# Kernel tuning notes

Measured on AMD Instinct MI355X. Metric: run time of the kernel, lower is better.

## Reference

```python
import jax, jax.numpy as jnp
import numpy as np

B, S, E, NH = 2, 2048, 1024, 4
HD = E // NH  # 256


def setup_inputs() -> dict:
    key = jax.random.key(0)
    ks = jax.random.split(key, 8)
    return {
        "q": jax.random.normal(ks[0], (B, S, E), jnp.float32),
        "k": jax.random.normal(ks[1], (B, S, E), jnp.float32),
        "v": jax.random.normal(ks[2], (B, S, E), jnp.float32),
        # gate Dense params (kernel zero-init in the module; use small random for a nontrivial baseline)
        "igate_kernel": jax.random.normal(ks[3], (3 * E, NH), jnp.float32) * 0.02,
        "igate_bias": jax.random.normal(ks[4], (NH,), jnp.float32) * 0.1,
        "fgate_kernel": jax.random.normal(ks[5], (3 * E, NH), jnp.float32) * 0.02,
        "fgate_bias": jnp.linspace(3.0, 6.0, NH, dtype=jnp.float32),  # bias_linspace_init
        "rms_scale": jax.random.normal(ks[6], (HD,), jnp.float32) * 0.02,
    }


def _mlstm_head(q, k, v, ig, fg, eps=1e-06):
    # q,k,v: (S, DH); ig, fg: (S, 1)
    s, dh = q.shape
    log_f = jax.nn.log_sigmoid(fg)                       # (S,1)
    cs = jnp.concatenate([jnp.zeros((1, 1), log_f.dtype),
                          jnp.cumsum(log_f, axis=0)], axis=0)  # (S+1,1)
    neg = jnp.asarray(-0.7 * jnp.finfo(cs.dtype).max, cs.dtype)
    log_d = jnp.where(jnp.tri(s, dtype=bool),
                      (cs - cs.T)[1:, 1:] + ig.T, neg)   # (S,S)
    m = jnp.max(log_d, axis=-1, keepdims=True)           # row-wise stabilizer
    d = jnp.exp(log_d - m)
    c = (q @ (k.T / jnp.sqrt(dh))) * d                   # (S,S)
    n = jnp.maximum(jnp.sum(c, axis=-1, keepdims=True), jnp.exp(-m))
    return (c / (n + eps)) @ v                           # (S,DH)


def reference(q, k, v, igate_kernel, igate_bias, fgate_kernel, fgate_bias, rms_scale):
    b, s, e = q.shape
    nh = igate_kernel.shape[1]
    hd = e // nh
    gate_in = jnp.concatenate((q, k, v), axis=-1)                 # (B,S,3E)
    ig = (gate_in @ igate_kernel + igate_bias).swapaxes(-1, -2)[..., None]  # (B,NH,S,1)
    fg = (gate_in @ fgate_kernel + fgate_bias).swapaxes(-1, -2)[..., None]  # (B,NH,S,1)
    qh = q.reshape(b, s, nh, hd).swapaxes(1, 2)                   # (B,NH,S,HD)
    kh = k.reshape(b, s, nh, hd).swapaxes(1, 2)
    vh = v.reshape(b, s, nh, hd).swapaxes(1, 2)
    h = jax.vmap(jax.vmap(_mlstm_head))(qh, kh, vh, ig, fg)      # (B,NH,S,HD)
    # RMSNorm over head_dim with (1+scale)
    var = jnp.mean(jnp.square(h.astype(jnp.float32)), axis=-1, keepdims=True)
    h = (h * jax.lax.rsqrt(var + 1e-06)).astype(h.dtype) * (1.0 + rms_scale)
    return h.swapaxes(1, 2).reshape(b, s, e)
```

## Files before the change

### kernel.cpp

```cpp
#include <hip/hip_runtime.h>
#include <math.h>

static constexpr int B_  = 2;
static constexpr int S_  = 2048;
static constexpr int E_  = 1024;
static constexpr int NH_ = 4;
static constexpr int HD_ = 256;
static constexpr int BH_ = B_ * NH_;

typedef __attribute__((ext_vector_type(8))) _Float16 half8;
typedef __attribute__((ext_vector_type(4))) float    f32x4;
typedef __attribute__((ext_vector_type(4))) _Float16 half4v;


__device__ __forceinline__ int wofs(int e) { return (e << 4) ^ ((e & 0x38) << 1); }

__global__ __launch_bounds__(1024) void prep_kernel(
    const float* __restrict__ q, const float* __restrict__ k, const float* __restrict__ v,
    const float* __restrict__ igk, const float* __restrict__ igb,
    const float* __restrict__ fgk, const float* __restrict__ fgb,
    float* __restrict__ ig_out, float* __restrict__ fg_out,
    _Float16* __restrict__ Qh, _Float16* __restrict__ Kh, _Float16* __restrict__ Vt)
{
    __shared__ __align__(16) char PSM[98304];
// ... 23 lines not shown
        const int e4 = l * 4 + 256 * j;
        float4 g4;
        if (j < 4)       g4 = *(const float4*)(qrow + e4);
        else if (j < 8)  g4 = *(const float4*)(krow + (e4 - E_));
        else             g4 = *(const float4*)(vrow + (e4 - 2 * E_));
        const float ge[4] = {g4.x, g4.y, g4.z, g4.w};
        if (j < 4) {
            const int d = e4 & 255, hh = e4 >> 8;
            const int idx = ((s >> 4) * 8 + (d >> 5)) * 512
                          + (s & 15) * 8 + (((d & 31) >> 3) << 7) + (d & 7);
            half4v st;
            st.x = (_Float16)(ge[0] * 0.0625f); st.y = (_Float16)(ge[1] * 0.0625f);
            st.z = (_Float16)(ge[2] * 0.0625f); st.w = (_Float16)(ge[3] * 0.0625f);
            *(half4v*)(Qh + ((size_t)(b * NH_ + hh)) * (S_ * HD_) + idx) = st;
        } else if (j < 8) {
            const int e2 = e4 - E_;
            const int d = e2 & 255, hh = e2 >> 8;
            const int idx = ((s >> 4) * 8 + (d >> 5)) * 512
                          + (s & 15) * 8 + (((d & 31) >> 3) << 7) + (d & 7);
            half4v st;
            st.x = (_Float16)ge[0]; st.y = (_Float16)ge[1];
            st.z = (_Float16)ge[2]; st.w = (_Float16)ge[3];
            *(half4v*)(Kh + ((size_t)(b * NH_ + hh)) * (S_ * HD_) + idx) = st;
        }
        #pragma unroll
        for (int i = 0; i < 4; ++i) {
            float4 wiv = *(const float4*)(wiB + wofs(e4 + i));
            float4 wfv = *(const float4*)(wfB + wofs(e4 + i));
            accI[0] = fmaf(ge[i], wiv.x, accI[0]); accI[1] = fmaf(ge[i], wiv.y, accI[1]);
            accI[2] = fmaf(ge[i], wiv.z, accI[2]); accI[3] = fmaf(ge[i], wiv.w, accI[3]);
            accF[0] = fmaf(ge[i], wfv.x, accF[0]); accF[1] = fmaf(ge[i], wfv.y, accF[1]);
            accF[2] = fmaf(ge[i], wfv.z, accF[2]); accF[3] = fmaf(ge[i], wfv.w, accF[3]);
        }
    }
    #pragma unroll
    for (int m = 1; m < 64; m <<= 1) {
        #pragma unroll
        for (int h = 0; h < 4; ++h) {
            accI[h] += __shfl_xor(accI[h], m);
            accF[h] += __shfl_xor(accF[h], m);
        }
    }
    if (l == 0) {
        #pragma unroll
        for (int h = 0; h < 4; ++h) {
            ig_out[((size_t)(b * NH_ + h)) * S_ + s] = accI[h] + igb[h];
            fg_out[((size_t)(b * NH_ + h)) * S_ + s] = accF[h] + fgb[h];
        }
    }

    __syncthreads();
    {
        float (*tile)[65] = (float(*)[65])(PSM + (t >> 8) * 16640);
        const int tid = t & 255;
        const int m  = blockIdx.x * 4 + (t >> 8);
        const int bh = m & 7;
        const int sb = (m >> 3) & 31;
        const int db = m >> 8;
        const int bb = bh >> 2, hh = bh & 3;
        const int j4 = (tid & 15) * 4;
        const int i0 = tid >> 4;
        const float* src = v + ((size_t)(bb * S_ + sb * 64)) * E_ + hh * HD_ + db * 64;
        #pragma unroll
        for (int p = 0; p < 4; ++p) {
            int i = i0 + p * 16;
            float4 val = *(const float4*)(src + (size_t)i * E_ + j4);
            tile[i][j4] = val.x; tile[i][j4+1] = val.y; tile[i][j4+2] = val.z; tile[i][j4+3] = val.w;
        }
        __syncthreads();
        const int ll = tid & 63;
        const int sw_ = tid >> 6;
        _Float16* dstb = Vt + (size_t)bh * (S_ * HD_);
        #pragma unroll
        for (int kb = 0; kb < 2; ++kb) {
            half8 pk;
            #pragma unroll
            for (int jj = 0; jj < 8; ++jj)
                pk[jj] = (_Float16)tile[kb * 32 + (ll >> 4) * 8 + jj][sw_ * 16 + (ll & 15)];
            *(half8*)(dstb + ((size_t)((sb * 16 + db * 4 + sw_) * 2 + kb)) * 512 + ll * 8) = pk;
        }
    }
}

static constexpr int OFF_AMM = 16384;
static constexpr int OFF_G   = OFF_AMM + S_ * 4;
static constexpr int OFF_M   = OFF_G + S_ * 4;
static constexpr int OFF_RS  = OFF_M + S_ * 4;
static constexpr int OFF_SS  = OFF_RS + 1024;
static constexpr int OFF_WR  = OFF_SS + 1024;
static constexpr int SMB     = OFF_WR + 64;

#define TILE_BODY(KFC, KFN)                                                   \
{                                                                             \
                  \
    const _Float16* vb_ = Vtp + (size_t)jt * 32768 + l * 8;                   \
    _Pragma("unroll")                                                         \
    for (int dn = 0; dn < 2; ++dn) {                                          \
        _Pragma("unroll")                                                     \
        for (int k0 = 0; k0 < 4; ++k0)                                        \
            vf[dn * 4 + k0] = *(const half8*)(vb_                             \
                + (((k0 >> 1) * 16 + w * 2 + dn) * 2 + (k0 & 1)) * 512);      \
    }                                                                         \
           \
    if (jt + 1 < Tt) {                                                        \
        const _Float16* kb_ = Kp + ((size_t)((jt + 1) * 8 + w) * 8) * 512 + l * 8; \
        _Pragma("unroll")                                                     \
        for (int kk = 0; kk < 8; ++kk)                                        \
            KFN[kk] = *(const half8*)(kb_ + kk * 512);                        \
    }                                                                         \
                                     \
    f32x4 sc0 = (f32x4){0.f,0.f,0.f,0.f}, sc1 = (f32x4){0.f,0.f,0.f,0.f};     \
    _Pragma("unroll")                                                         \
    for (int kk = 0; kk < 8; ++kk) {                                          \
        sc0 = __builtin_amdgcn_mfma_f32_16x16x32_f16(qf0[kk], KFC[kk], sc0, 0, 0, 0); \
        sc1 = __builtin_amdgcn_mfma_f32_16x16x32_f16(qf1[kk], KFC[kk], sc1, 0, 0, 0); \
    }                                                                         \
     \
    const int gcol = jt * 128 + w * 16 + col;                                 \
    const float gv = sG[gcol];                                                \
    char* pbC = Pb + buf * 8192;                                              \
    const int pcb = (w * 16 + col) * 2;                                       \
    _Pragma("unroll")                                                         \
    for (int rr = 0; rr < 4; ++rr) {                                          \
        const int r0 = quad * 4 + rr;                                         \
        const int sw = (r0 & 7) << 4;                                         \
        float e0 = __expf(amM0[rr] + gv);                                     \
        float p0 = (gcol <= rowbase + r0) ? sc0[rr] * e0 : 0.f;               \
        rs0[rr] += p0;                                                        \
        *(_Float16*)(pbC + r0 * 256 + (pcb ^ sw)) = (_Float16)p0;             \
        float e1 = __expf(amM1[rr] + gv);                                     \
        float p1 = (gcol <= rowbase + 16 + r0) ? sc1[rr] * e1 : 0.f;          \
        rs1[rr] += p1;                                                        \
        *(_Float16*)(pbC + (r0 + 16) * 256 + (pcb ^ sw)) = (_Float16)p1;      \
    }                                                                         \
     \
    asm volatile("s_waitcnt lgkmcnt(0)" ::: "memory");                        \
    __builtin_amdgcn_s_barrier();                                             \
     \
    _Pragma("unroll")                                                         \
    for (int rsub = 0; rsub < 2; ++rsub) {                                    \
        const char* base = pbC + (rsub * 16 + col) * 256;                     \
        const int sw2 = (col & 7) << 4;                                       \
        half8 af[4];                                                          \
        _Pragma("unroll")                                                     \
        for (int k0 = 0; k0 < 4; ++k0)                                        \
            af[k0] = *(const half8*)(base + ((k0 * 64 + quad * 16) ^ sw2));   \
        _Pragma("unroll")                                                     \
        for (int k0 = 0; k0 < 4; ++k0) {                                      \
            acc[rsub * 2 + 0] = __builtin_amdgcn_mfma_f32_16x16x32_f16(af[k0], vf[k0],     acc[rsub * 2 + 0], 0, 0, 0); \
            acc[rsub * 2 + 1] = __builtin_amdgcn_mfma_f32_16x16x32_f16(af[k0], vf[4 + k0], acc[rsub * 2 + 1], 0, 0, 0); \
        }                                                                     \
    }                                                                         \
    buf ^= 1;                                                                 \
}

__global__ __launch_bounds__(512, 2) void mlstm_kernel(
    const _Float16* __restrict__ Qh, const _Float16* __restrict__ Kh,
    const _Float16* __restrict__ Vt,
    const float* __restrict__ ig, const float* __restrict__ fg,
    const float* __restrict__ rms_scale, float* __restrict__ out)
{
    __shared__ __align__(16) char SMEM[SMB];
    char*  Pb    = SMEM;
    float* sAmM  = (float*)(SMEM + OFF_AMM);
    float* sG    = (float*)(SMEM + OFF_G);
    float* sM    = (float*)(SMEM + OFF_M);
    float* rsumP = (float*)(SMEM + OFF_RS);
    float* ssP   = (float*)(SMEM + OFF_SS);
    float* wred  = (float*)(SMEM + OFF_WR);
    float* wred2 = wred + 8;

    const int z  = blockIdx.x;
    const int bh = z & 7;
    const int u  = (z >> 3) & 31;
    const int pass = z >> 8;
    const int b  = bh >> 2, h = bh & 3;
    const int t  = threadIdx.x;
    const int w  = t >> 6;
    const int l  = t & 63;
    const int col  = l & 15;
    const int quad = l >> 4;

    {
        const float* fgp = fg + (size_t)bh * S_;
        const float* igp = ig + (size_t)bh * S_;
        float4 fx = *(const float4*)(fgp + t * 4);
        float4 ix = *(const float4*)(igp + t * 4);
        float xi[4] = {fx.x, fx.y, fx.z, fx.w};
        float gi[4] = {ix.x, ix.y, ix.z, ix.w};
        float ls[4];
        float run = 0.f;
        #pragma unroll
        for (int i = 0; i < 4; ++i) {
            float x = xi[i];
            float lg = (x >= 0.f) ? -log1pf(expf(-x)) : (x - log1pf(expf(x)));
            run += lg;
            ls[i] = run;
        }
        const float own = run;
        #pragma unroll
        for (int m = 1; m < 64; m <<= 1) {
            float o = __shfl_up(run, m);
            if (l >= m) run += o;
        }
        if (l == 63) wred[w] = run;
        __syncthreads();
        float wpre = 0.f;
        for (int ww = 0; ww < w; ++ww) wpre += wred[ww];
        const float exclT = wpre + run - own;
        float A[4], g[4], gm[4];
        float rmax = -__builtin_inff();
        #pragma unroll
        for (int i = 0; i < 4; ++i) {
            A[i] = exclT + ls[i];
            g[i] = gi[i] - A[i];
            rmax = fmaxf(rmax, g[i]);
            gm[i] = rmax;
        }
        float sm = rmax;
        #pragma unroll
        for (int m = 1; m < 64; m <<= 1) {
            float o = __shfl_up(sm, m);
            if (l >= m) sm = fmaxf(sm, o);
        }
        if (l == 63) wred2[w] = sm;
        __syncthreads();
        float exm = -__builtin_inff();
        for (int ww = 0; ww < w; ++ww) exm = fmaxf(exm, wred2[ww]);
        float up = __shfl_up(sm, 1);
        if (l > 0) exm = fmaxf(exm, up);
        #pragma unroll
        for (int i = 0; i < 4; ++i) {
            float cm = fmaxf(exm, gm[i]);
            float Mi = A[i] + cm;
            sAmM[t * 4 + i] = A[i] - Mi;
            sG[t * 4 + i]   = g[i];
            sM[t * 4 + i]   = Mi;
        }
        __syncthreads();
    }

    const _Float16* Qp  = Qh + (size_t)bh * S_ * HD_;
    const _Float16* Kp  = Kh + (size_t)bh * S_ * HD_;
    const _Float16* Vtp = Vt + (size_t)bh * HD_ * S_;

    const int rb = pass ? (63 - u) : u;
    const int rowbase = rb * 32;
    const int Tt = (rb >> 2) + 1;

    half8 qf0[8], qf1[8];
    {
        const _Float16* qb0 = Qp + ((size_t)(rb * 2) * 8) * 512 + l * 8;
        const _Float16* qb1 = Qp + ((size_t)(rb * 2 + 1) * 8) * 512 + l * 8;
        #pragma unroll
        for (int kk = 0; kk < 8; ++kk) {
            qf0[kk] = *(const half8*)(qb0 + kk * 512);
            qf1[kk] = *(const half8*)(qb1 + kk * 512);
        }
    }
    float amM0[4], amM1[4];
    #pragma unroll
    for (int rr = 0; rr < 4; ++rr) {
        amM0[rr] = sAmM[rowbase + quad * 4 + rr];
        amM1[rr] = sAmM[rowbase + 16 + quad * 4 + rr];
    }

    f32x4 acc[4];
    #pragma unroll
    for (int i = 0; i < 4; ++i) acc[i] = (f32x4){0.f, 0.f, 0.f, 0.f};
    float rs0[4] = {0.f,0.f,0.f,0.f}, rs1[4] = {0.f,0.f,0.f,0.f};

    half8 kf0[8], kf1[8], vf[8];
    {
        const _Float16* kb_ = Kp + ((size_t)(w * 8)) * 512 + l * 8;
        #pragma unroll
        for (int kk = 0; kk < 8; ++kk)
            kf0[kk] = *(const half8*)(kb_ + kk * 512);
    }

    int buf = 0;
    int jt = 0;
    while (true) {
        TILE_BODY(kf0, kf1);
        if (++jt >= Tt) break;
        TILE_BODY(kf1, kf0);
        if (++jt >= Tt) break;
    }

    #pragma unroll
    for (int m = 1; m < 16; m <<= 1) {
        #pragma unroll
        for (int rr = 0; rr < 4; ++rr) {
            rs0[rr] += __shfl_xor(rs0[rr], m);
            rs1[rr] += __shfl_xor(rs1[rr], m);
        }
    }
    if (col == 0) {
        #pragma unroll
        for (int rr = 0; rr < 4; ++rr) {
            rsumP[w * 32 + quad * 4 + rr]      = rs0[rr];
            rsumP[w * 32 + 16 + quad * 4 + rr] = rs1[rr];
        }
    }
    __syncthreads();
    float inv0[4], inv1[4];
    #pragma unroll
    for (int rr = 0; rr < 4; ++rr) {
        const int r0 = quad * 4 + rr;
        float tot0 = 0.f, tot1 = 0.f;
        #pragma unroll
        for (int ww = 0; ww < 8; ++ww) {
            tot0 += rsumP[ww * 32 + r0];
            tot1 += rsumP[ww * 32 + 16 + r0];
        }
        float M0 = sM[rowbase + r0];
        float M1 = sM[rowbase + 16 + r0];
        inv0[rr] = 1.0f / (fmaxf(tot0, __expf(-M0)) + 1e-6f);
        inv1[rr] = 1.0f / (fmaxf(tot1, __expf(-M1)) + 1e-6f);
    }
    float ss0[4] = {0.f,0.f,0.f,0.f}, ss1[4] = {0.f,0.f,0.f,0.f};
    #pragma unroll
    for (int dn = 0; dn < 2; ++dn) {
        #pragma unroll
        for (int rr = 0; rr < 4; ++rr) {
            float h0 = acc[dn][rr] * inv0[rr];
            acc[dn][rr] = h0;
            ss0[rr] = fmaf(h0, h0, ss0[rr]);
            float h1 = acc[2 + dn][rr] * inv1[rr];
            acc[2 + dn][rr] = h1;
            ss1[rr] = fmaf(h1, h1, ss1[rr]);
        }
    }
    #pragma unroll
    for (int m = 1; m < 16; m <<= 1) {
        #pragma unroll
        for (int rr = 0; rr < 4; ++rr) {
            ss0[rr] += __shfl_xor(ss0[rr], m);
            ss1[rr] += __shfl_xor(ss1[rr], m);
        }
    }
    if (col == 0) {
        #pragma unroll
        for (int rr = 0; rr < 4; ++rr) {
            ssP[w * 32 + quad * 4 + rr]      = ss0[rr];
            ssP[w * 32 + 16 + quad * 4 + rr] = ss1[rr];
        }
    }
    __syncthreads();
    const float rsc0 = 1.f + rms_scale[w * 32 + col];
    const float rsc1 = 1.f + rms_scale[w * 32 + 16 + col];
    #pragma unroll
    for (int rr = 0; rr < 4; ++rr) {
        const int r0 = quad * 4 + rr;
        float sst0 = 0.f, sst1 = 0.f;
        #pragma unroll
        for (int ww = 0; ww < 8; ++ww) {
            sst0 += ssP[ww * 32 + r0];
            sst1 += ssP[ww * 32 + 16 + r0];
        }
        float rstd0 = rsqrtf(sst0 * (1.0f / HD_) + 1e-6f);
        float rstd1 = rsqrtf(sst1 * (1.0f / HD_) + 1e-6f);
        float* o0 = out + ((size_t)(b * S_ + rowbase + r0)) * E_ + h * HD_ + w * 32;
        float* o1 = out + ((size_t)(b * S_ + rowbase + 16 + r0)) * E_ + h * HD_ + w * 32;
        o0[col]      = acc[0][rr] * rstd0 * rsc0;
        o0[16 + col] = acc[1][rr] * rstd0 * rsc1;
        o1[col]      = acc[2][rr] * rstd1 * rsc0;
        o1[16 + col] = acc[3][rr] * rstd1 * rsc1;
    }
}

extern "C" void kernel_launch(void* const* d_in, const int* in_sizes, int n_in,
                              void* d_out, int out_size, void* d_ws, size_t ws_size,
                              hipStream_t stream) {
    (void)in_sizes; (void)n_in; (void)out_size; (void)ws_size;
    const float* q   = (const float*)d_in[0];
    const float* k   = (const float*)d_in[1];
    const float* v   = (const float*)d_in[2];
    const float* igk = (const float*)d_in[3];
    const float* igb = (const float*)d_in[4];
    const float* fgk = (const float*)d_in[5];
    const float* fgb = (const float*)d_in[6];
    const float* rsc = (const float*)d_in[7];
    float* out = (float*)d_out;

    float* ws  = (float*)d_ws;
    float* ig  = ws;
    float* fg  = ws + (size_t)BH_ * S_;
    _Float16* Qh = (_Float16*)(ws + (size_t)2 * BH_ * S_);
    _Float16* Kh = Qh + (size_t)BH_ * S_ * HD_;
    _Float16* Vt = Kh + (size_t)BH_ * S_ * HD_;

    prep_kernel<<<B_ * S_ / 16, 1024, 0, stream>>>(q, k, v, igk, igb, fgk, fgb,
                                                   ig, fg, Qh, Kh, Vt);
    mlstm_kernel<<<BH_ * 64, 512, 0, stream>>>(Qh, Kh, Vt, ig, fg, rsc, out);
}
```

Measured before the change: 161.1 us.

## Software-pipeline QK and PV across tiles with transposed scores and exp2

Restructures the attention main loop so that the QK^T MFMAs for tile j+1 run alongside the PV MFMAs for tile j, with V and K loads issued after the matrix work and one barrier per iteration. Scores are now computed transposed (K as the A operand), so each lane holds four consecutive columns for one row. This lets the P tile be written as packed half4 stores and row sums be reduced with two shuffles instead of four. Gates are pre-scaled by log2(e) so the hardware exp2 can replace expf, masking is applied only on the diagonal tile, and s_setprio raises wave priority around the MFMA blocks. The cost is more complex control flow with peeled prologue and epilogue, and possibly higher register pressure from the overlapping live ranges.

```diff
diff --git a/kernel.cpp b/kernel.cpp
--- a/kernel.cpp
+++ b/kernel.cpp
@@ -137,70 +137,6 @@
 static constexpr int OFF_WR  = OFF_SS + 1024;
 static constexpr int SMB     = OFF_WR + 64;
 
-#define TILE_BODY(KFC, KFN)                                                   \
-{                                                                             \
-                  \
-    const _Float16* vb_ = Vtp + (size_t)jt * 32768 + l * 8;                   \
-    _Pragma("unroll")                                                         \
-    for (int dn = 0; dn < 2; ++dn) {                                          \
-        _Pragma("unroll")                                                     \
-        for (int k0 = 0; k0 < 4; ++k0)                                        \
-            vf[dn * 4 + k0] = *(const half8*)(vb_                             \
-                + (((k0 >> 1) * 16 + w * 2 + dn) * 2 + (k0 & 1)) * 512);      \
-    }                                                                         \
-           \
-    if (jt + 1 < Tt) {                                                        \
-        const _Float16* kb_ = Kp + ((size_t)((jt + 1) * 8 + w) * 8) * 512 + l * 8; \
-        _Pragma("unroll")                                                     \
-        for (int kk = 0; kk < 8; ++kk)                                        \
-            KFN[kk] = *(const half8*)(kb_ + kk * 512);                        \
-    }                                                                         \
-                                     \
-    f32x4 sc0 = (f32x4){0.f,0.f,0.f,0.f}, sc1 = (f32x4){0.f,0.f,0.f,0.f};     \
-    _Pragma("unroll")                                                         \
-    for (int kk = 0; kk < 8; ++kk) {                                          \
-        sc0 = __builtin_amdgcn_mfma_f32_16x16x32_f16(qf0[kk], KFC[kk], sc0, 0, 0, 0); \
-        sc1 = __builtin_amdgcn_mfma_f32_16x16x32_f16(qf1[kk], KFC[kk], sc1, 0, 0, 0); \
-    }                                                                         \
-     \
-    const int gcol = jt * 128 + w * 16 + col;                                 \
-    const float gv = sG[gcol];                                                \
-    char* pbC = Pb + buf * 8192;                                              \
-    const int pcb = (w * 16 + col) * 2;                                       \
-    _Pragma("unroll")                                                         \
-    for (int rr = 0; rr < 4; ++rr) {                                          \
-        const int r0 = quad * 4 + rr;                                         \
-        const int sw = (r0 & 7) << 4;                                         \
-        float e0 = __expf(amM0[rr] + gv);                                     \
-        float p0 = (gcol <= rowbase + r0) ? sc0[rr] * e0 : 0.f;               \
-        rs0[rr] += p0;                                                        \
-        *(_Float16*)(pbC + r0 * 256 + (pcb ^ sw)) = (_Float16)p0;             \
-        float e1 = __expf(amM1[rr] + gv);                                     \
-        float p1 = (gcol <= rowbase + 16 + r0) ? sc1[rr] * e1 : 0.f;          \
-        rs1[rr] += p1;                                                        \
-        *(_Float16*)(pbC + (r0 + 16) * 256 + (pcb ^ sw)) = (_Float16)p1;      \
-    }                                                                         \
-     \
-    asm volatile("s_waitcnt lgkmcnt(0)" ::: "memory");                        \
-    __builtin_amdgcn_s_barrier();                                             \
-     \
-    _Pragma("unroll")                                                         \
-    for (int rsub = 0; rsub < 2; ++rsub) {                                    \
-        const char* base = pbC + (rsub * 16 + col) * 256;                     \
-        const int sw2 = (col & 7) << 4;                                       \
-        half8 af[4];                                                          \
-        _Pragma("unroll")                                                     \
-        for (int k0 = 0; k0 < 4; ++k0)                                        \
-            af[k0] = *(const half8*)(base + ((k0 * 64 + quad * 16) ^ sw2));   \
-        _Pragma("unroll")                                                     \
-        for (int k0 = 0; k0 < 4; ++k0) {                                      \
-            acc[rsub * 2 + 0] = __builtin_amdgcn_mfma_f32_16x16x32_f16(af[k0], vf[k0],     acc[rsub * 2 + 0], 0, 0, 0); \
-            acc[rsub * 2 + 1] = __builtin_amdgcn_mfma_f32_16x16x32_f16(af[k0], vf[4 + k0], acc[rsub * 2 + 1], 0, 0, 0); \
-        }                                                                     \
-    }                                                                         \
-    buf ^= 1;                                                                 \
-}
-
 __global__ __launch_bounds__(512, 2) void mlstm_kernel(
     const _Float16* __restrict__ Qh, const _Float16* __restrict__ Kh,
     const _Float16* __restrict__ Vt,
@@ -227,6 +163,7 @@
     const int l  = t & 63;
     const int col  = l & 15;
     const int quad = l >> 4;
+    constexpr float LOG2E = 1.4426950408889634f;
 
     {
         const float* fgp = fg + (size_t)bh * S_;
@@ -280,8 +217,8 @@
         for (int i = 0; i < 4; ++i) {
             float cm = fmaxf(exm, gm[i]);
             float Mi = A[i] + cm;
-            sAmM[t * 4 + i] = A[i] - Mi;
-            sG[t * 4 + i]   = g[i];
+            sAmM[t * 4 + i] = (A[i] - Mi) * LOG2E;
+            sG[t * 4 + i]   = g[i] * LOG2E;
             sM[t * 4 + i]   = Mi;
         }
         __syncthreads();
@@ -305,49 +242,142 @@
             qf1[kk] = *(const half8*)(qb1 + kk * 512);
         }
     }
-    float amM0[4], amM1[4];
-    #pragma unroll
-    for (int rr = 0; rr < 4; ++rr) {
-        amM0[rr] = sAmM[rowbase + quad * 4 + rr];
-        amM1[rr] = sAmM[rowbase + 16 + quad * 4 + rr];
-    }
+    const float amM0 = sAmM[rowbase + col];
+    const float amM1 = sAmM[rowbase + 16 + col];
 
     f32x4 acc[4];
     #pragma unroll
     for (int i = 0; i < 4; ++i) acc[i] = (f32x4){0.f, 0.f, 0.f, 0.f};
-    float rs0[4] = {0.f,0.f,0.f,0.f}, rs1[4] = {0.f,0.f,0.f,0.f};
-
-    half8 kf0[8], kf1[8], vf[8];
+    float rs0 = 0.f, rs1 = 0.f;
+
+    half8 kfA[8], kfB[8], vf[8];
+
+    auto ISSK = [&](half8* KN, int tile) {
+        const _Float16* kb_ = Kp + ((size_t)(tile * 8 + w) * 8) * 512 + l * 8;
+        #pragma unroll
+        for (int kk = 0; kk < 8; ++kk)
+            KN[kk] = *(const half8*)(kb_ + kk * 512);
+    };
+    auto ISSV = [&](int tile) {
+        const _Float16* vb_ = Vtp + (size_t)tile * 32768 + l * 8;
+        #pragma unroll
+        for (int dn = 0; dn < 2; ++dn) {
+            #pragma unroll
+            for (int k0 = 0; k0 < 4; ++k0)
+                vf[dn * 4 + k0] = *(const half8*)(vb_
+                    + (((k0 >> 1) * 16 + w * 2 + dn) * 2 + (k0 & 1)) * 512);
+        }
+    };
+    auto QK = [&](const half8* KC, f32x4& s0, f32x4& s1) {
+        #pragma unroll
+        for (int kk = 0; kk < 8; ++kk) {
+            s0 = __builtin_amdgcn_mfma_f32_16x16x32_f16(KC[kk], qf0[kk], s0, 0, 0, 0);
+            s1 = __builtin_amdgcn_mfma_f32_16x16x32_f16(KC[kk], qf1[kk], s1, 0, 0, 0);
+        }
+    };
+    auto PV = [&](int bufo) {
+        const char* pbC = Pb + bufo;
+        const int sw2 = (col & 7) << 4;
+        #pragma unroll
+        for (int rsub = 0; rsub < 2; ++rsub) {
+            const char* base = pbC + (rsub * 16 + col) * 256;
+            half8 af[4];
+            #pragma unroll
+            for (int k0 = 0; k0 < 4; ++k0)
+                af[k0] = *(const half8*)(base + ((k0 * 64 + quad * 16) ^ sw2));
+            #pragma unroll
+            for (int k0 = 0; k0 < 4; ++k0) {
+                acc[rsub * 2 + 0] = __builtin_amdgcn_mfma_f32_16x16x32_f16(af[k0], vf[k0],     acc[rsub * 2 + 0], 0, 0, 0);
+                acc[rsub * 2 + 1] = __builtin_amdgcn_mfma_f32_16x16x32_f16(af[k0], vf[4 + k0], acc[rsub * 2 + 1], 0, 0, 0);
+            }
+        }
+    };
+    auto FIXUP = [&](int jt, int bufo, bool MASKED, const f32x4& s0, const f32x4& s1) {
+        float4 gv4 = *(const float4*)(sG + jt * 128 + w * 16 + quad * 4);
+        const float gvv[4] = {gv4.x, gv4.y, gv4.z, gv4.w};
+        half4v h0, h1;
+        #pragma unroll
+        for (int rr = 0; rr < 4; ++rr) {
+            float p0 = s0[rr] * __builtin_amdgcn_exp2f(amM0 + gvv[rr]);
+            float p1 = s1[rr] * __builtin_amdgcn_exp2f(amM1 + gvv[rr]);
+            if (MASKED) {
+                const int gc = jt * 128 + w * 16 + quad * 4 + rr;
+                p0 = (gc <= rowbase + col) ? p0 : 0.f;
+                p1 = (gc <= rowbase + 16 + col) ? p1 : 0.f;
+            }
+            rs0 += p0; rs1 += p1;
+            h0[rr] = (_Float16)p0;
+            h1[rr] = (_Float16)p1;
+        }
+        char* pbC = Pb + bufo;
+        const int wb = (w * 32 + quad * 8) ^ ((col & 7) << 4);
+        *(half4v*)(pbC + col * 256 + wb) = h0;
+        *(half4v*)(pbC + (16 + col) * 256 + wb) = h1;
+    };
+
+    ISSK(kfA, 0);
+    ISSV(0);
+    if (Tt > 1) ISSK(kfB, 1);
     {
-        const _Float16* kb_ = Kp + ((size_t)(w * 8)) * 512 + l * 8;
-        #pragma unroll
-        for (int kk = 0; kk < 8; ++kk)
-            kf0[kk] = *(const half8*)(kb_ + kk * 512);
-    }
-
-    int buf = 0;
-    int jt = 0;
-    while (true) {
-        TILE_BODY(kf0, kf1);
-        if (++jt >= Tt) break;
-        TILE_BODY(kf1, kf0);
-        if (++jt >= Tt) break;
-    }
-
-    #pragma unroll
-    for (int m = 1; m < 16; m <<= 1) {
-        #pragma unroll
-        for (int rr = 0; rr < 4; ++rr) {
-            rs0[rr] += __shfl_xor(rs0[rr], m);
-            rs1[rr] += __shfl_xor(rs1[rr], m);
-        }
-    }
-    if (col == 0) {
-        #pragma unroll
-        for (int rr = 0; rr < 4; ++rr) {
-            rsumP[w * 32 + quad * 4 + rr]      = rs0[rr];
-            rsumP[w * 32 + 16 + quad * 4 + rr] = rs1[rr];
-        }
+        f32x4 s0 = (f32x4){0.f,0.f,0.f,0.f}, s1 = (f32x4){0.f,0.f,0.f,0.f};
+        QK(kfA, s0, s1);
+        if (Tt == 1) FIXUP(0, 0, true, s0, s1);
+        else         FIXUP(0, 0, false, s0, s1);
+    }
+    asm volatile("s_waitcnt lgkmcnt(0)" ::: "memory");
+    __builtin_amdgcn_s_barrier();
+
+    int j = 0;
+    while (j + 2 < Tt) {
+        {
+            f32x4 s0 = (f32x4){0.f,0.f,0.f,0.f}, s1 = (f32x4){0.f,0.f,0.f,0.f};
+            __builtin_amdgcn_s_setprio(1);
+            QK(kfB, s0, s1);
+            PV((j & 1) * 8192);
+            __builtin_amdgcn_s_setprio(0);
+            ISSV(j + 1);
+            ISSK(kfA, j + 2);
+            FIXUP(j + 1, ((j + 1) & 1) * 8192, false, s0, s1);
+            asm volatile("s_waitcnt lgkmcnt(0)" ::: "memory");
+            __builtin_amdgcn_s_barrier();
+            ++j;
+        }
+        if (!(j + 2 < Tt)) break;
+        {
+            f32x4 s0 = (f32x4){0.f,0.f,0.f,0.f}, s1 = (f32x4){0.f,0.f,0.f,0.f};
+            __builtin_amdgcn_s_setprio(1);
+            QK(kfA, s0, s1);
+            PV((j & 1) * 8192);
+            __builtin_amdgcn_s_setprio(0);
+            ISSV(j + 1);
+            ISSK(kfB, j + 2);
+            FIXUP(j + 1, ((j + 1) & 1) * 8192, false, s0, s1);
+            asm volatile("s_waitcnt lgkmcnt(0)" ::: "memory");
+            __builtin_amdgcn_s_barrier();
+            ++j;
+        }
+    }
+    if (Tt >= 2) {
+        f32x4 s0 = (f32x4){0.f,0.f,0.f,0.f}, s1 = (f32x4){0.f,0.f,0.f,0.f};
+        __builtin_amdgcn_s_setprio(1);
+        if ((Tt - 1) & 1) QK(kfB, s0, s1);
+        else              QK(kfA, s0, s1);
+        PV((j & 1) * 8192);
+        __builtin_amdgcn_s_setprio(0);
+        ISSV(Tt - 1);
+        FIXUP(Tt - 1, ((Tt - 1) & 1) * 8192, true, s0, s1);
+        asm volatile("s_waitcnt lgkmcnt(0)" ::: "memory");
+        __builtin_amdgcn_s_barrier();
+    }
+    __builtin_amdgcn_s_setprio(1);
+    PV(((Tt - 1) & 1) * 8192);
+    __builtin_amdgcn_s_setprio(0);
+
+    rs0 += __shfl_xor(rs0, 16); rs0 += __shfl_xor(rs0, 32);
+    rs1 += __shfl_xor(rs1, 16); rs1 += __shfl_xor(rs1, 32);
+    if (quad == 0) {
+        rsumP[w * 32 + col]      = rs0;
+        rsumP[w * 32 + 16 + col] = rs1;
     }
     __syncthreads();
     float inv0[4], inv1[4];
```

Measured after the change: 201.5 us. 1.25x slower.

## Transpose score MFMA, peel masked diagonal tile, use exp2 and setprio

Applied to the files above, without the earlier changes.

The score MFMA now takes its operands swapped, so each lane owns one query row (col) and four key columns. That allows one row-stabilizer per lane, a single vector load of the gate values, packed half4 stores of P, and a shorter row-sum reduction. The causal mask is only applied in a peeled final diagonal tile, and the gate and log terms are prescaled by log2(e) so the hardware exp2 can be used. s_setprio is raised around the MFMA sections to favour matrix issue. The changes add code-size duplication from the extra TILE_BODY instance and change rounding slightly.

```diff
diff --git a/kernel.cpp b/kernel.cpp
--- a/kernel.cpp
+++ b/kernel.cpp
@@ -137,66 +137,79 @@
 static constexpr int OFF_WR  = OFF_SS + 1024;
 static constexpr int SMB     = OFF_WR + 64;
 
-#define TILE_BODY(KFC, KFN)                                                   \
+#define TILE_BODY(KFC, KFN, MASKED)                                           \
 {                                                                             \
                   \
-    const _Float16* vb_ = Vtp + (size_t)jt * 32768 + l * 8;                   \
-    _Pragma("unroll")                                                         \
-    for (int dn = 0; dn < 2; ++dn) {                                          \
+    {                                                                         \
+        const _Float16* vb_ = Vtp + (size_t)jt * 32768 + l * 8;               \
         _Pragma("unroll")                                                     \
-        for (int k0 = 0; k0 < 4; ++k0)                                        \
-            vf[dn * 4 + k0] = *(const half8*)(vb_                             \
-                + (((k0 >> 1) * 16 + w * 2 + dn) * 2 + (k0 & 1)) * 512);      \
+        for (int dn = 0; dn < 2; ++dn) {                                      \
+            _Pragma("unroll")                                                 \
+            for (int k0 = 0; k0 < 4; ++k0)                                    \
+                vf[dn * 4 + k0] = *(const half8*)(vb_                         \
+                    + (((k0 >> 1) * 16 + w * 2 + dn) * 2 + (k0 & 1)) * 512);  \
+        }                                                                     \
     }                                                                         \
            \
-    if (jt + 1 < Tt) {                                                        \
+    if (!MASKED) {                                                            \
         const _Float16* kb_ = Kp + ((size_t)((jt + 1) * 8 + w) * 8) * 512 + l * 8; \
         _Pragma("unroll")                                                     \
         for (int kk = 0; kk < 8; ++kk)                                        \
             KFN[kk] = *(const half8*)(kb_ + kk * 512);                        \
     }                                                                         \
-                                     \
-    f32x4 sc0 = (f32x4){0.f,0.f,0.f,0.f}, sc1 = (f32x4){0.f,0.f,0.f,0.f};     \
+         \
+    f32x4 s0 = (f32x4){0.f,0.f,0.f,0.f}, s1 = (f32x4){0.f,0.f,0.f,0.f};      \
+    __builtin_amdgcn_s_setprio(1);                                            \
     _Pragma("unroll")                                                         \
     for (int kk = 0; kk < 8; ++kk) {                                          \
-        sc0 = __builtin_amdgcn_mfma_f32_16x16x32_f16(qf0[kk], KFC[kk], sc0, 0, 0, 0); \
-        sc1 = __builtin_amdgcn_mfma_f32_16x16x32_f16(qf1[kk], KFC[kk], sc1, 0, 0, 0); \
+        s0 = __builtin_amdgcn_mfma_f32_16x16x32_f16(KFC[kk], qf0[kk], s0, 0, 0, 0); \
+        s1 = __builtin_amdgcn_mfma_f32_16x16x32_f16(KFC[kk], qf1[kk], s1, 0, 0, 0); \
     }                                                                         \
-     \
-    const int gcol = jt * 128 + w * 16 + col;                                 \
-    const float gv = sG[gcol];                                                \
-    char* pbC = Pb + buf * 8192;                                              \
-    const int pcb = (w * 16 + col) * 2;                                       \
-    _Pragma("unroll")                                                         \
-    for (int rr = 0; rr < 4; ++rr) {                                          \
-        const int r0 = quad * 4 + rr;                                         \
-        const int sw = (r0 & 7) << 4;                                         \
-        float e0 = __expf(amM0[rr] + gv);                                     \
-        float p0 = (gcol <= rowbase + r0) ? sc0[rr] * e0 : 0.f;               \
-        rs0[rr] += p0;                                                        \
-        *(_Float16*)(pbC + r0 * 256 + (pcb ^ sw)) = (_Float16)p0;             \
-        float e1 = __expf(amM1[rr] + gv);                                     \
-        float p1 = (gcol <= rowbase + 16 + r0) ? sc1[rr] * e1 : 0.f;          \
-        rs1[rr] += p1;                                                        \
-        *(_Float16*)(pbC + (r0 + 16) * 256 + (pcb ^ sw)) = (_Float16)p1;      \
+    __builtin_amdgcn_s_setprio(0);                                            \
+         \
+    {                                                                         \
+        float4 gv4 = *(const float4*)(sG + jt * 128 + w * 16 + quad * 4);     \
+        const float gvv[4] = {gv4.x, gv4.y, gv4.z, gv4.w};                    \
+        char* pbC = Pb + buf * 8192;                                          \
+        half4v h0, h1;                                                        \
+        _Pragma("unroll")                                                     \
+        for (int rr = 0; rr < 4; ++rr) {                                      \
+            float p0 = s0[rr] * __builtin_amdgcn_exp2f(amM0 + gvv[rr]);       \
+            float p1 = s1[rr] * __builtin_amdgcn_exp2f(amM1 + gvv[rr]);       \
+            if (MASKED) {                                                     \
+                const int gc = jt * 128 + w * 16 + quad * 4 + rr;             \
+                p0 = (gc <= rowbase + col) ? p0 : 0.f;                        \
+                p1 = (gc <= rowbase + 16 + col) ? p1 : 0.f;                   \
+            }                                                                 \
+            rs0 += p0; rs1 += p1;                                             \
+            h0[rr] = (_Float16)p0; h1[rr] = (_Float16)p1;                     \
+        }                                                                     \
+        const int wb = (w * 32 + quad * 8) ^ ((col & 7) << 4);                \
+        *(half4v*)(pbC + col * 256 + wb) = h0;                                \
+        *(half4v*)(pbC + (16 + col) * 256 + wb) = h1;                         \
     }                                                                         \
      \
     asm volatile("s_waitcnt lgkmcnt(0)" ::: "memory");                        \
     __builtin_amdgcn_s_barrier();                                             \
      \
-    _Pragma("unroll")                                                         \
-    for (int rsub = 0; rsub < 2; ++rsub) {                                    \
-        const char* base = pbC + (rsub * 16 + col) * 256;                     \
+    {                                                                         \
+        const char* pbC = Pb + buf * 8192;                                    \
         const int sw2 = (col & 7) << 4;                                       \
-        half8 af[4];                                                          \
+        __builtin_amdgcn_s_setprio(1);                                        \
         _Pragma("unroll")                                                     \
-        for (int k0 = 0; k0 < 4; ++k0)                                        \
-            af[k0] = *(const half8*)(base + ((k0 * 64 + quad * 16) ^ sw2));   \
-        _Pragma("unroll")                                                     \
-        for (int k0 = 0; k0 < 4; ++k0) {                                      \
-            acc[rsub * 2 + 0] = __builtin_amdgcn_mfma_f32_16x16x32_f16(af[k0], vf[k0],     acc[rsub * 2 + 0], 0, 0, 0); \
-            acc[rsub * 2 + 1] = __builtin_amdgcn_mfma_f32_16x16x32_f16(af[k0], vf[4 + k0], acc[rsub * 2 + 1], 0, 0, 0); \
+        for (int rsub = 0; rsub < 2; ++rsub) {                                \
+            const char* base = pbC + (rsub * 16 + col) * 256;                 \
+            half8 af[4];                                                      \
+            _Pragma("unroll")                                                 \
+            for (int k0 = 0; k0 < 4; ++k0)                                    \
+                af[k0] = *(const half8*)(base + ((k0 * 64 + quad * 16) ^ sw2)); \
+            _Pragma("unroll")                                                 \
+            for (int k0 = 0; k0 < 4; ++k0) {                                  \
+                acc[rsub * 2 + 0] = __builtin_amdgcn_mfma_f32_16x16x32_f16(af[k0], vf[k0],     acc[rsub * 2 + 0], 0, 0, 0); \
+                acc[rsub * 2 + 1] = __builtin_amdgcn_mfma_f32_16x16x32_f16(af[k0], vf[4 + k0], acc[rsub * 2 + 1], 0, 0, 0); \
+            }                                                                 \
         }                                                                     \
+        __builtin_amdgcn_s_setprio(0);                                        \
     }                                                                         \
     buf ^= 1;                                                                 \
 }
@@ -227,6 +240,7 @@
     const int l  = t & 63;
     const int col  = l & 15;
     const int quad = l >> 4;
+    constexpr float LOG2E = 1.4426950408889634f;
 
     {
         const float* fgp = fg + (size_t)bh * S_;
@@ -280,8 +294,8 @@
         for (int i = 0; i < 4; ++i) {
             float cm = fmaxf(exm, gm[i]);
             float Mi = A[i] + cm;
-            sAmM[t * 4 + i] = A[i] - Mi;
-            sG[t * 4 + i]   = g[i];
+            sAmM[t * 4 + i] = (A[i] - Mi) * LOG2E;
+            sG[t * 4 + i]   = g[i] * LOG2E;
             sM[t * 4 + i]   = Mi;
         }
         __syncthreads();
@@ -305,49 +319,38 @@
             qf1[kk] = *(const half8*)(qb1 + kk * 512);
         }
     }
-    float amM0[4], amM1[4];
-    #pragma unroll
-    for (int rr = 0; rr < 4; ++rr) {
-        amM0[rr] = sAmM[rowbase + quad * 4 + rr];
-        amM1[rr] = sAmM[rowbase + 16 + quad * 4 + rr];
-    }
+    const float amM0 = sAmM[rowbase + col];
+    const float amM1 = sAmM[rowbase + 16 + col];
 
     f32x4 acc[4];
     #pragma unroll
     for (int i = 0; i < 4; ++i) acc[i] = (f32x4){0.f, 0.f, 0.f, 0.f};
-    float rs0[4] = {0.f,0.f,0.f,0.f}, rs1[4] = {0.f,0.f,0.f,0.f};
-
-    half8 kf0[8], kf1[8], vf[8];
+    float rs0 = 0.f, rs1 = 0.f;
+
+    half8 kfA[8], kfB[8], vf[8];
     {
         const _Float16* kb_ = Kp + ((size_t)(w * 8)) * 512 + l * 8;
         #pragma unroll
         for (int kk = 0; kk < 8; ++kk)
-            kf0[kk] = *(const half8*)(kb_ + kk * 512);
+            kfA[kk] = *(const half8*)(kb_ + kk * 512);
     }
 
     int buf = 0;
     int jt = 0;
-    while (true) {
-        TILE_BODY(kf0, kf1);
-        if (++jt >= Tt) break;
-        TILE_BODY(kf1, kf0);
-        if (++jt >= Tt) break;
-    }
-
-    #pragma unroll
-    for (int m = 1; m < 16; m <<= 1) {
-        #pragma unroll
-        for (int rr = 0; rr < 4; ++rr) {
-            rs0[rr] += __shfl_xor(rs0[rr], m);
-            rs1[rr] += __shfl_xor(rs1[rr], m);
-        }
-    }
-    if (col == 0) {
-        #pragma unroll
-        for (int rr = 0; rr < 4; ++rr) {
-            rsumP[w * 32 + quad * 4 + rr]      = rs0[rr];
-            rsumP[w * 32 + 16 + quad * 4 + rr] = rs1[rr];
-        }
+    while (jt + 1 < Tt) {
+        TILE_BODY(kfA, kfB, false);
+        if (++jt + 1 >= Tt) break;
+        TILE_BODY(kfB, kfA, false);
+        ++jt;
+    }
+    if (jt & 1) { TILE_BODY(kfB, kfA, true); }
+    else        { TILE_BODY(kfA, kfB, true); }
+
+    rs0 += __shfl_xor(rs0, 16); rs0 += __shfl_xor(rs0, 32);
+    rs1 += __shfl_xor(rs1, 16); rs1 += __shfl_xor(rs1, 32);
+    if (quad == 0) {
+        rsumP[w * 32 + col]      = rs0;
+        rsumP[w * 32 + 16 + col] = rs1;
     }
     __syncthreads();
     float inv0[4], inv1[4];
```

Result: slower. 164.9 us (+2.4%).

## Warp-specialize mLSTM kernel into QK and PV producer/consumer waves

Applied to the files above, without the earlier changes.

Splits each block into 1024 threads: eight waves compute QK scores and gated probabilities, while eight other waves load V and run the PV matmul one tile behind, pipelined through double-buffered shared memory. Each block now handles both the light and heavy row-block pass in a loop, so the grid is halved. Q is staged in LDS instead of registers, exp is switched to exp2 with log2e prescaled gates, the causal mask is applied only on the diagonal tile, and output stores are nontemporal. The aim is to overlap the two matmul phases and cut register pressure, at the cost of more barriers per tile and less parallelism across blocks.

```diff
diff --git a/kernel.cpp b/kernel.cpp
--- a/kernel.cpp
+++ b/kernel.cpp
@@ -129,65 +129,75 @@
     }
 }
 
-static constexpr int OFF_AMM = 16384;
+static constexpr int OFF_PB  = 16384;
+static constexpr int OFF_AMM = OFF_PB + 16384;
 static constexpr int OFF_G   = OFF_AMM + S_ * 4;
 static constexpr int OFF_M   = OFF_G + S_ * 4;
 static constexpr int OFF_RS  = OFF_M + S_ * 4;
 static constexpr int OFF_SS  = OFF_RS + 1024;
 static constexpr int OFF_WR  = OFF_SS + 1024;
-static constexpr int SMB     = OFF_WR + 64;
-
-#define TILE_BODY(KFC, KFN)                                                   \
+static constexpr int SMB     = OFF_WR + 128;
+
+#define QK_BODY(ii)                                                           \
 {                                                                             \
-                  \
-    const _Float16* vb_ = Vtp + (size_t)jt * 32768 + l * 8;                   \
+    const int ii_ = (ii);                                                     \
+    f32x4 s0 = (f32x4){0.f,0.f,0.f,0.f}, s1 = (f32x4){0.f,0.f,0.f,0.f};      \
+    __builtin_amdgcn_s_setprio(1);                                            \
+    _Pragma("unroll")                                                         \
+    for (int kk = 0; kk < 8; ++kk) {                                          \
+        half8 q0 = *(const half8*)(qlds + (kk * 64 + l) * 16);                \
+        half8 q1 = *(const half8*)(qlds + 8192 + (kk * 64 + l) * 16);         \
+        s0 = __builtin_amdgcn_mfma_f32_16x16x32_f16(kf[kk], q0, s0, 0, 0, 0); \
+        s1 = __builtin_amdgcn_mfma_f32_16x16x32_f16(kf[kk], q1, s1, 0, 0, 0); \
+    }                                                                         \
+    __builtin_amdgcn_s_setprio(0);                                            \
+    if (ii_ + 1 < Tt) {      \
+        const _Float16* kb_ = Kp + ((size_t)((ii_ + 1) * 8 + wp) * 8) * 512 + l * 8; \
+        _Pragma("unroll")                                                     \
+        for (int kk = 0; kk < 8; ++kk) kf[kk] = *(const half8*)(kb_ + kk * 512); \
+    }                                                                         \
+    float4 gv4 = *(const float4*)(sG + ii_ * 128 + wp * 16 + quad * 4);       \
+    const float gvv[4] = {gv4.x, gv4.y, gv4.z, gv4.w};                        \
+    char* pbC = Pb + (ii_ & 1) * 8192;                                        \
+    half4v h0, h1;                                                            \
+    const bool mask_ = (ii_ == Tt - 1);                                       \
+    _Pragma("unroll")                                                         \
+    for (int rr = 0; rr < 4; ++rr) {                                          \
+        float p0 = s0[rr] * __builtin_amdgcn_exp2f(amM0 + gvv[rr]);           \
+        float p1 = s1[rr] * __builtin_amdgcn_exp2f(amM1 + gvv[rr]);           \
+        if (mask_) {                                                          \
+            const int gc = ii_ * 128 + wp * 16 + quad * 4 + rr;               \
+            p0 = (gc <= rowbase + col) ? p0 : 0.f;                            \
+            p1 = (gc <= rowbase + 16 + col) ? p1 : 0.f;                       \
+        }                                                                     \
+        rs0 += p0; rs1 += p1;                                                 \
+        h0[rr] = (_Float16)p0; h1[rr] = (_Float16)p1;                         \
+    }                                                                         \
+    const int wb = (wp * 32 + quad * 8) ^ ((col & 7) << 4);                   \
+    *(half4v*)(pbC + col * 256 + wb) = h0;                                    \
+    *(half4v*)(pbC + (16 + col) * 256 + wb) = h1;                             \
+}
+
+#define ISSV(jj)                                                              \
+{                                                                             \
+    const _Float16* vb_ = Vtp + (size_t)(jj) * 32768 + l * 8;                 \
     _Pragma("unroll")                                                         \
     for (int dn = 0; dn < 2; ++dn) {                                          \
         _Pragma("unroll")                                                     \
         for (int k0 = 0; k0 < 4; ++k0)                                        \
             vf[dn * 4 + k0] = *(const half8*)(vb_                             \
-                + (((k0 >> 1) * 16 + w * 2 + dn) * 2 + (k0 & 1)) * 512);      \
+                + (((k0 >> 1) * 16 + wp * 2 + dn) * 2 + (k0 & 1)) * 512);     \
     }                                                                         \
-           \
-    if (jt + 1 < Tt) {                                                        \
-        const _Float16* kb_ = Kp + ((size_t)((jt + 1) * 8 + w) * 8) * 512 + l * 8; \
-        _Pragma("unroll")                                                     \
-        for (int kk = 0; kk < 8; ++kk)                                        \
-            KFN[kk] = *(const half8*)(kb_ + kk * 512);                        \
-    }                                                                         \
-                                     \
-    f32x4 sc0 = (f32x4){0.f,0.f,0.f,0.f}, sc1 = (f32x4){0.f,0.f,0.f,0.f};     \
-    _Pragma("unroll")                                                         \
-    for (int kk = 0; kk < 8; ++kk) {                                          \
-        sc0 = __builtin_amdgcn_mfma_f32_16x16x32_f16(qf0[kk], KFC[kk], sc0, 0, 0, 0); \
-        sc1 = __builtin_amdgcn_mfma_f32_16x16x32_f16(qf1[kk], KFC[kk], sc1, 0, 0, 0); \
-    }                                                                         \
-     \
-    const int gcol = jt * 128 + w * 16 + col;                                 \
-    const float gv = sG[gcol];                                                \
-    char* pbC = Pb + buf * 8192;                                              \
-    const int pcb = (w * 16 + col) * 2;                                       \
-    _Pragma("unroll")                                                         \
-    for (int rr = 0; rr < 4; ++rr) {                                          \
-        const int r0 = quad * 4 + rr;                                         \
-        const int sw = (r0 & 7) << 4;                                         \
-        float e0 = __expf(amM0[rr] + gv);                                     \
-        float p0 = (gcol <= rowbase + r0) ? sc0[rr] * e0 : 0.f;               \
-        rs0[rr] += p0;                                                        \
-        *(_Float16*)(pbC + r0 * 256 + (pcb ^ sw)) = (_Float16)p0;             \
-        float e1 = __expf(amM1[rr] + gv);                                     \
-        float p1 = (gcol <= rowbase + 16 + r0) ? sc1[rr] * e1 : 0.f;          \
-        rs1[rr] += p1;                                                        \
-        *(_Float16*)(pbC + (r0 + 16) * 256 + (pcb ^ sw)) = (_Float16)p1;      \
-    }                                                                         \
-     \
-    asm volatile("s_waitcnt lgkmcnt(0)" ::: "memory");                        \
-    __builtin_amdgcn_s_barrier();                                             \
-     \
+}
+
+#define PV_BODY(jj)                                                           \
+{                                                                             \
+    const char* pbC = Pb + ((jj) & 1) * 8192;                                 \
+    const int sw2 = (col & 7) << 4;                                           \
+    __builtin_amdgcn_s_setprio(1);                                            \
     _Pragma("unroll")                                                         \
     for (int rsub = 0; rsub < 2; ++rsub) {                                    \
         const char* base = pbC + (rsub * 16 + col) * 256;                     \
-        const int sw2 = (col & 7) << 4;                                       \
         half8 af[4];                                                          \
         _Pragma("unroll")                                                     \
         for (int k0 = 0; k0 < 4; ++k0)                                        \
@@ -198,47 +208,55 @@
             acc[rsub * 2 + 1] = __builtin_amdgcn_mfma_f32_16x16x32_f16(af[k0], vf[4 + k0], acc[rsub * 2 + 1], 0, 0, 0); \
         }                                                                     \
     }                                                                         \
-    buf ^= 1;                                                                 \
-}
-
-__global__ __launch_bounds__(512, 2) void mlstm_kernel(
+    __builtin_amdgcn_s_setprio(0);                                            \
+}
+
+#define LGKM_BARRIER() do {                                                   \
+    asm volatile("s_waitcnt lgkmcnt(0)" ::: "memory");                        \
+    __builtin_amdgcn_s_barrier();                                             \
+} while (0)
+
+__global__ __launch_bounds__(1024, 4) void mlstm_kernel(
     const _Float16* __restrict__ Qh, const _Float16* __restrict__ Kh,
     const _Float16* __restrict__ Vt,
     const float* __restrict__ ig, const float* __restrict__ fg,
     const float* __restrict__ rms_scale, float* __restrict__ out)
 {
     __shared__ __align__(16) char SMEM[SMB];
-    char*  Pb    = SMEM;
+    char*  qlds  = SMEM;
+    char*  Pb    = SMEM + OFF_PB;
     float* sAmM  = (float*)(SMEM + OFF_AMM);
     float* sG    = (float*)(SMEM + OFF_G);
     float* sM    = (float*)(SMEM + OFF_M);
     float* rsumP = (float*)(SMEM + OFF_RS);
     float* ssP   = (float*)(SMEM + OFF_SS);
     float* wred  = (float*)(SMEM + OFF_WR);
-    float* wred2 = wred + 8;
+    float* wred2 = wred + 16;
 
     const int z  = blockIdx.x;
     const int bh = z & 7;
-    const int u  = (z >> 3) & 31;
-    const int pass = z >> 8;
+    const int u  = z >> 3;
     const int b  = bh >> 2, h = bh & 3;
     const int t  = threadIdx.x;
     const int w  = t >> 6;
     const int l  = t & 63;
     const int col  = l & 15;
     const int quad = l >> 4;
+    const bool isQK = (w < 8);
+    const int wp = w & 7;
+    constexpr float LOG2E = 1.4426950408889634f;
 
     {
         const float* fgp = fg + (size_t)bh * S_;
         const float* igp = ig + (size_t)bh * S_;
-        float4 fx = *(const float4*)(fgp + t * 4);
-        float4 ix = *(const float4*)(igp + t * 4);
-        float xi[4] = {fx.x, fx.y, fx.z, fx.w};
-        float gi[4] = {ix.x, ix.y, ix.z, ix.w};
-        float ls[4];
+        float2 fx = *(const float2*)(fgp + t * 2);
+        float2 ix = *(const float2*)(igp + t * 2);
+        float xi[2] = {fx.x, fx.y};
+        float gi[2] = {ix.x, ix.y};
+        float ls[2];
         float run = 0.f;
         #pragma unroll
-        for (int i = 0; i < 4; ++i) {
+        for (int i = 0; i < 2; ++i) {
             float x = xi[i];
             float lg = (x >= 0.f) ? -log1pf(expf(-x)) : (x - log1pf(expf(x)));
             run += lg;
@@ -255,10 +273,10 @@
         float wpre = 0.f;
         for (int ww = 0; ww < w; ++ww) wpre += wred[ww];
         const float exclT = wpre + run - own;
-        float A[4], g[4], gm[4];
+        float A[2], g[2], gm[2];
         float rmax = -__builtin_inff();
         #pragma unroll
-        for (int i = 0; i < 4; ++i) {
+        for (int i = 0; i < 2; ++i) {
             A[i] = exclT + ls[i];
             g[i] = gi[i] - A[i];
             rmax = fmaxf(rmax, g[i]);
@@ -277,12 +295,12 @@
         float up = __shfl_up(sm, 1);
         if (l > 0) exm = fmaxf(exm, up);
         #pragma unroll
-        for (int i = 0; i < 4; ++i) {
+        for (int i = 0; i < 2; ++i) {
             float cm = fmaxf(exm, gm[i]);
             float Mi = A[i] + cm;
-            sAmM[t * 4 + i] = A[i] - Mi;
-            sG[t * 4 + i]   = g[i];
-            sM[t * 4 + i]   = Mi;
+            sAmM[t * 2 + i] = (A[i] - Mi) * LOG2E;
+            sG[t * 2 + i]   = g[i] * LOG2E;
+            sM[t * 2 + i]   = Mi;
         }
         __syncthreads();
     }
@@ -291,128 +309,124 @@
     const _Float16* Kp  = Kh + (size_t)bh * S_ * HD_;
     const _Float16* Vtp = Vt + (size_t)bh * HD_ * S_;
 
-    const int rb = pass ? (63 - u) : u;
-    const int rowbase = rb * 32;
-    const int Tt = (rb >> 2) + 1;
-
-    half8 qf0[8], qf1[8];
-    {
-        const _Float16* qb0 = Qp + ((size_t)(rb * 2) * 8) * 512 + l * 8;
-        const _Float16* qb1 = Qp + ((size_t)(rb * 2 + 1) * 8) * 512 + l * 8;
-        #pragma unroll
-        for (int kk = 0; kk < 8; ++kk) {
-            qf0[kk] = *(const half8*)(qb0 + kk * 512);
-            qf1[kk] = *(const half8*)(qb1 + kk * 512);
-        }
-    }
-    float amM0[4], amM1[4];
-    #pragma unroll
-    for (int rr = 0; rr < 4; ++rr) {
-        amM0[rr] = sAmM[rowbase + quad * 4 + rr];
-        amM1[rr] = sAmM[rowbase + 16 + quad * 4 + rr];
-    }
-
-    f32x4 acc[4];
-    #pragma unroll
-    for (int i = 0; i < 4; ++i) acc[i] = (f32x4){0.f, 0.f, 0.f, 0.f};
-    float rs0[4] = {0.f,0.f,0.f,0.f}, rs1[4] = {0.f,0.f,0.f,0.f};
-
-    half8 kf0[8], kf1[8], vf[8];
-    {
-        const _Float16* kb_ = Kp + ((size_t)(w * 8)) * 512 + l * 8;
-        #pragma unroll
-        for (int kk = 0; kk < 8; ++kk)
-            kf0[kk] = *(const half8*)(kb_ + kk * 512);
-    }
-
-    int buf = 0;
-    int jt = 0;
-    while (true) {
-        TILE_BODY(kf0, kf1);
-        if (++jt >= Tt) break;
-        TILE_BODY(kf1, kf0);
-        if (++jt >= Tt) break;
-    }
-
-    #pragma unroll
-    for (int m = 1; m < 16; m <<= 1) {
-        #pragma unroll
-        for (int rr = 0; rr < 4; ++rr) {
-            rs0[rr] += __shfl_xor(rs0[rr], m);
-            rs1[rr] += __shfl_xor(rs1[rr], m);
-        }
-    }
-    if (col == 0) {
-        #pragma unroll
-        for (int rr = 0; rr < 4; ++rr) {
-            rsumP[w * 32 + quad * 4 + rr]      = rs0[rr];
-            rsumP[w * 32 + 16 + quad * 4 + rr] = rs1[rr];
-        }
-    }
-    __syncthreads();
-    float inv0[4], inv1[4];
-    #pragma unroll
-    for (int rr = 0; rr < 4; ++rr) {
-        const int r0 = quad * 4 + rr;
-        float tot0 = 0.f, tot1 = 0.f;
-        #pragma unroll
-        for (int ww = 0; ww < 8; ++ww) {
-            tot0 += rsumP[ww * 32 + r0];
-            tot1 += rsumP[ww * 32 + 16 + r0];
-        }
-        float M0 = sM[rowbase + r0];
-        float M1 = sM[rowbase + 16 + r0];
-        inv0[rr] = 1.0f / (fmaxf(tot0, __expf(-M0)) + 1e-6f);
-        inv1[rr] = 1.0f / (fmaxf(tot1, __expf(-M1)) + 1e-6f);
-    }
-    float ss0[4] = {0.f,0.f,0.f,0.f}, ss1[4] = {0.f,0.f,0.f,0.f};
-    #pragma unroll
-    for (int dn = 0; dn < 2; ++dn) {
-        #pragma unroll
-        for (int rr = 0; rr < 4; ++rr) {
-            float h0 = acc[dn][rr] * inv0[rr];
-            acc[dn][rr] = h0;
-            ss0[rr] = fmaf(h0, h0, ss0[rr]);
-            float h1 = acc[2 + dn][rr] * inv1[rr];
-            acc[2 + dn][rr] = h1;
-            ss1[rr] = fmaf(h1, h1, ss1[rr]);
-        }
-    }
-    #pragma unroll
-    for (int m = 1; m < 16; m <<= 1) {
-        #pragma unroll
-        for (int rr = 0; rr < 4; ++rr) {
-            ss0[rr] += __shfl_xor(ss0[rr], m);
-            ss1[rr] += __shfl_xor(ss1[rr], m);
-        }
-    }
-    if (col == 0) {
-        #pragma unroll
-        for (int rr = 0; rr < 4; ++rr) {
-            ssP[w * 32 + quad * 4 + rr]      = ss0[rr];
-            ssP[w * 32 + 16 + quad * 4 + rr] = ss1[rr];
-        }
-    }
-    __syncthreads();
-    const float rsc0 = 1.f + rms_scale[w * 32 + col];
-    const float rsc1 = 1.f + rms_scale[w * 32 + 16 + col];
-    #pragma unroll
-    for (int rr = 0; rr < 4; ++rr) {
-        const int r0 = quad * 4 + rr;
-        float sst0 = 0.f, sst1 = 0.f;
-        #pragma unroll
-        for (int ww = 0; ww < 8; ++ww) {
-            sst0 += ssP[ww * 32 + r0];
-            sst1 += ssP[ww * 32 + 16 + r0];
-        }
-        float rstd0 = rsqrtf(sst0 * (1.0f / HD_) + 1e-6f);
-        float rstd1 = rsqrtf(sst1 * (1.0f / HD_) + 1e-6f);
-        float* o0 = out + ((size_t)(b * S_ + rowbase + r0)) * E_ + h * HD_ + w * 32;
-        float* o1 = out + ((size_t)(b * S_ + rowbase + 16 + r0)) * E_ + h * HD_ + w * 32;
-        o0[col]      = acc[0][rr] * rstd0 * rsc0;
-        o0[16 + col] = acc[1][rr] * rstd0 * rsc1;
-        o1[col]      = acc[2][rr] * rstd1 * rsc0;
-        o1[16 + col] = acc[3][rr] * rstd1 * rsc1;
+    half8 kf[8], vf[8];
+
+    for (int pass = 0; pass < 2; ++pass) {
+        const int rb = pass ? (63 - u) : u;
+        const int rowbase = rb * 32;
+        const int Tt = (rb >> 2) + 1;
+
+        {
+            const _Float16* qsrc = Qp + ((size_t)(rb * 16 + (t >> 6))) * 512 + (t & 63) * 8;
+            *(half8*)(qlds + t * 16) = *(const half8*)qsrc;
+        }
+        float amM0 = 0.f, amM1 = 0.f, rs0 = 0.f, rs1 = 0.f;
+        f32x4 acc[4];
+        if (isQK) {
+            const _Float16* kb_ = Kp + ((size_t)(wp * 8)) * 512 + l * 8;
+            #pragma unroll
+            for (int kk = 0; kk < 8; ++kk)
+                kf[kk] = *(const half8*)(kb_ + kk * 512);
+            amM0 = sAmM[rowbase + col];
+            amM1 = sAmM[rowbase + 16 + col];
+        } else {
+            #pragma unroll
+            for (int i = 0; i < 4; ++i) acc[i] = (f32x4){0.f, 0.f, 0.f, 0.f};
+        }
+        LGKM_BARRIER();
+
+        if (isQK) { QK_BODY(0); }
+        else      { ISSV(0); }
+        LGKM_BARRIER();
+        for (int i = 1; ; ++i) {
+            if (isQK) {
+                if (i < Tt) QK_BODY(i);
+            } else {
+                PV_BODY(i - 1);
+                if (i < Tt) ISSV(i);
+            }
+            LGKM_BARRIER();
+            if (i >= Tt) break;
+        }
+
+        if (isQK) {
+            rs0 += __shfl_xor(rs0, 16); rs0 += __shfl_xor(rs0, 32);
+            rs1 += __shfl_xor(rs1, 16); rs1 += __shfl_xor(rs1, 32);
+            if (quad == 0) {
+                rsumP[wp * 32 + col]      = rs0;
+                rsumP[wp * 32 + 16 + col] = rs1;
+            }
+        }
+        __syncthreads();
+        if (!isQK) {
+            float inv0[4], inv1[4];
+            #pragma unroll
+            for (int rr = 0; rr < 4; ++rr) {
+                const int r0 = quad * 4 + rr;
+                float tot0 = 0.f, tot1 = 0.f;
+                #pragma unroll
+                for (int ww = 0; ww < 8; ++ww) {
+                    tot0 += rsumP[ww * 32 + r0];
+                    tot1 += rsumP[ww * 32 + 16 + r0];
+                }
+                float M0 = sM[rowbase + r0];
+                float M1 = sM[rowbase + 16 + r0];
+                inv0[rr] = 1.0f / (fmaxf(tot0, __expf(-M0)) + 1e-6f);
+                inv1[rr] = 1.0f / (fmaxf(tot1, __expf(-M1)) + 1e-6f);
+            }
+            float ss0[4] = {0.f,0.f,0.f,0.f}, ss1[4] = {0.f,0.f,0.f,0.f};
+            #pragma unroll
+            for (int dn = 0; dn < 2; ++dn) {
+                #pragma unroll
+                for (int rr = 0; rr < 4; ++rr) {
+                    float h0 = acc[dn][rr] * inv0[rr];
+                    acc[dn][rr] = h0;
+                    ss0[rr] = fmaf(h0, h0, ss0[rr]);
+                    float h1 = acc[2 + dn][rr] * inv1[rr];
+                    acc[2 + dn][rr] = h1;
+                    ss1[rr] = fmaf(h1, h1, ss1[rr]);
+                }
+            }
+            #pragma unroll
+            for (int m = 1; m < 16; m <<= 1) {
+                #pragma unroll
+                for (int rr = 0; rr < 4; ++rr) {
+                    ss0[rr] += __shfl_xor(ss0[rr], m);
+                    ss1[rr] += __shfl_xor(ss1[rr], m);
+                }
+            }
+            if (col == 0) {
+                #pragma unroll
+                for (int rr = 0; rr < 4; ++rr) {
+                    ssP[wp * 32 + quad * 4 + rr]      = ss0[rr];
+                    ssP[wp * 32 + 16 + quad * 4 + rr] = ss1[rr];
+                }
+            }
+        }
+        __syncthreads();
+        if (!isQK) {
+            const float rsc0 = 1.f + rms_scale[wp * 32 + col];
+            const float rsc1 = 1.f + rms_scale[wp * 32 + 16 + col];
+            #pragma unroll
+            for (int rr = 0; rr < 4; ++rr) {
+                const int r0 = quad * 4 + rr;
+                float sst0 = 0.f, sst1 = 0.f;
+                #pragma unroll
+                for (int ww = 0; ww < 8; ++ww) {
+                    sst0 += ssP[ww * 32 + r0];
+                    sst1 += ssP[ww * 32 + 16 + r0];
+                }
+                float rstd0 = rsqrtf(sst0 * (1.0f / HD_) + 1e-6f);
+                float rstd1 = rsqrtf(sst1 * (1.0f / HD_) + 1e-6f);
+                float* o0 = out + ((size_t)(b * S_ + rowbase + r0)) * E_ + h * HD_ + wp * 32;
+                float* o1 = out + ((size_t)(b * S_ + rowbase + 16 + r0)) * E_ + h * HD_ + wp * 32;
+                __builtin_nontemporal_store(acc[0][rr] * rstd0 * rsc0, o0 + col);
+                __builtin_nontemporal_store(acc[1][rr] * rstd0 * rsc1, o0 + 16 + col);
+                __builtin_nontemporal_store(acc[2][rr] * rstd1 * rsc0, o1 + col);
+                __builtin_nontemporal_store(acc[3][rr] * rstd1 * rsc1, o1 + 16 + col);
+            }
+        }
+        __syncthreads();
     }
 }
 
@@ -439,5 +453,5 @@
 
     prep_kernel<<<B_ * S_ / 16, 1024, 0, stream>>>(q, k, v, igk, igb, fgk, fgb,
                                                    ig, fg, Qh, Kh, Vt);
-    mlstm_kernel<<<BH_ * 64, 512, 0, stream>>>(Qh, Kh, Vt, ig, fg, rsc, out);
-}
+    mlstm_kernel<<<BH_ * 32, 1024, 0, stream>>>(Qh, Kh, Vt, ig, fg, rsc, out);
+}
```

Result: slower. 219.8 us (+36.4%).
